# Optimization experiments

Hardware: AMD Instinct MI355X
Metric: run time of the kernel (lower is better)

The kernel has to match this reference:

```python
import jax
import jax.numpy as jnp
import numpy as np

KSIZE, STRIDE, RATE, FUSE_K, SCALE = 3, 1, 2, 3, 10.0
ESCAPE_NAN = 1e-4


def _same_pad(x, k, s):
    # replicates torch same_padding: asymmetric zero pad so out = ceil(H/s)
    H, W = x.shape[2], x.shape[3]
    oh, ow = -(-H // s), -(-W // s)
    ph = max(0, (oh - 1) * s + k - H)
    pw = max(0, (ow - 1) * s + k - W)
    return jnp.pad(x, ((0, 0), (0, 0), (ph // 2, ph - ph // 2), (pw // 2, pw - pw // 2)))


def _extract_patches(x, k, s):
    # torch extract_image_patches: -> [B, L, C, k, k] with L = out_h*out_w
    x = _same_pad(x, k, s)
    B, C, H, W = x.shape
    Ho, Wo = (H - k) // s + 1, (W - k) // s + 1
    slices = [x[:, :, i:i + Ho * s:s, j:j + Wo * s:s] for i in range(k) for j in range(k)]
    p = jnp.stack(slices, axis=2).reshape(B, C, k, k, Ho, Wo)
    return p.transpose(0, 4, 5, 1, 2, 3).reshape(B, Ho * Wo, C, k, k)


def _contextual_attention(f, b, mask):
    dn = ('NCHW', 'OIHW', 'NCHW')
    # raw background patches for the final deconv: k = 2*rate, stride = rate
    raw_pat = _extract_patches(b, 2 * RATE, RATE * STRIDE)  # [B, L, C, 4, 4]
    # nearest-neighbor 1/rate downsample (torch F.interpolate nearest, sf=0.5)
    f_ds = f[:, :, ::RATE, ::RATE]
    b_ds = b[:, :, ::RATE, ::RATE]
    m_ds = mask[:, :, ::RATE, ::RATE]
    B, C, Hf, Wf = f_ds.shape
    Hb, Wb = b_ds.shape[2], b_ds.shape[3]
    b_pat = _extract_patches(b_ds, KSIZE, STRIDE)  # [B, L, C, 3, 3], L = Hb*Wb
    m_pat = _extract_patches(m_ds, KSIZE, STRIDE)[0]  # [L, 1, 3, 3] (first sample only, as in torch)
    mm = (jnp.mean(m_pat, axis=(1, 2, 3)) == 0.0).astype(f.dtype)[None, :, None, None]  # [1, L, 1, 1]
    fuse_w = jnp.eye(FUSE_K, dtype=f.dtype).reshape(1, 1, FUSE_K, FUSE_K)

    def per_item(xi, wi, raw_wi):
        # xi: [C,Hf,Wf]; wi: [L,C,3,3]; raw_wi: [L,C,4,4]
        max_wi = jnp.sqrt(jnp.sum(wi * wi + ESCAPE_NAN, axis=(1, 2, 3), keepdims=True))
        wi_n = wi / max_wi
        # matching conv: scores [1, L, Hf, Wf]
        yi = jax.lax.conv_general_dilated(xi[None], wi_n, (1, 1), ((1, 1), (1, 1)), dimension_numbers=dn)
        # fuse: identity-diagonal 3x3 conv along (bg_idx, fg_idx) twice with transposes
        yi = yi.reshape(1, 1, Hb * Wb, Hf * Wf)
        yi = jax.lax.conv_general_dilated(yi, fuse_w, (1, 1), ((1, 1), (1, 1)), dimension_numbers=dn)
        yi = yi.reshape(Hb, Wb, Hf, Wf).transpose(1, 0, 3, 2).reshape(1, 1, Hb * Wb, Hf * Wf)
        yi = jax.lax.conv_general_dilated(yi, fuse_w, (1, 1), ((1, 1), (1, 1)), dimension_numbers=dn)
        yi = yi.reshape(Wb, Hb, Wf, Hf).transpose(1, 0, 3, 2).reshape(1, Hb * Wb, Hf, Wf)
        yi = yi * mm
        yi = jax.nn.softmax(yi * SCALE, axis=1) * mm
        # conv_transpose2d(yi, raw_wi[I=L,O=C], stride=rate, padding=1) / 4
        w2 = jnp.flip(raw_wi, (2, 3)).transpose(1, 0, 2, 3)  # [C, L, 4, 4]
        pad = 2 * RATE - 1 - 1  # k - 1 - torch_padding = 2
        out = jax.lax.conv_general_dilated(yi, w2, (1, 1), ((pad, pad), (pad, pad)),
                                           lhs_dilation=(RATE, RATE), dimension_numbers=dn) / 4.0
        return out[0]

    return jax.vmap(per_item)(f_ds, b_pat, raw_pat)  # [B, C, H, W]


def setup_inputs() -> dict:
    key = jax.random.key(0)
    k1, k2 = jax.random.split(key)
    B, C, H, W = 2, 128, 128, 128
    f = jax.random.normal(k1, (B, C, H, W), dtype=jnp.float32)
    b = jax.random.normal(k2, (B, C, H, W), dtype=jnp.float32)
    mask = jnp.zeros((B, 1, H, W), dtype=jnp.float32)
    return {"f": f, "b": b, "mask": mask}


def reference(f, b, mask):
    return _contextual_attention(f, b, mask)
```

## Files before the change

### kernel.cpp

```cpp
#include <hip/hip_runtime.h>
#include <math.h>

#define CDIM 128
#define HF   128
#define WF   128
#define NP   4096
#define NCHUNK 64

typedef __attribute__((ext_vector_type(8))) short short8;
typedef float __attribute__((ext_vector_type(4), aligned(16))) f4a16;
typedef float __attribute__((ext_vector_type(4), aligned(4)))  f4u;

__device__ inline ushort f2bf(float x) {
  union { float f; unsigned u; } v; v.f = x;
  unsigned r = v.u + 0x7fff + ((v.u >> 16) & 1);
  return (ushort)(r >> 16);
}
__device__ inline float bf2f(ushort h) {
  union { unsigned u; float f; } v; v.u = ((unsigned)h) << 16; return v.f;
}

__device__ inline void gl2lds16(const ushort* g, ushort* l) {
  __builtin_amdgcn_global_load_lds((const __attribute__((address_space(1))) void*)g,
                                   (__attribute__((address_space(3))) void*)l, 16, 0, 0);
}

__global__ __launch_bounds__(256) void k_prep(const float* __restrict__ f,
                                              const float* __restrict__ b,
                                              ushort* __restrict__ fcat,
                                              ushort* __restrict__ bcat) {
  int idx = blockIdx.x * 256 + threadIdx.x;
  int c = idx & 127, pos = idx >> 7;
  int x = pos & 63, y = pos >> 6;
  int src = c * 16384 + y * 256 + x * 2;
  float fv = f[src], bv = b[src];
  ushort fh = f2bf(fv); ushort fl = f2bf(fv - bf2f(fh));
  ushort bh = f2bf(bv); ushort bl = f2bf(bv - bf2f(bh));
  size_t base = (size_t)pos * 384;
  fcat[base + c] = fh; fcat[base + 128 + c] = fl; fcat[base + 256 + c] = fh;
  bcat[base + c] = bh; bcat[base + 128 + c] = bh; bcat[base + 256 + c] = bl;
}

__global__ __launch_bounds__(256) void k_mmp(const float* __restrict__ mask,
                                             float* __restrict__ mmp) {
  int a = blockIdx.x * 256 + threadIdx.x;
  int yb = a & 63, xb = a >> 6;
  float s = 0.f;
  for (int dy = -1; dy <= 1; ++dy)
    for (int dx = -1; dx <= 1; ++dx) {
      int y = yb + dy, x = xb + dx;
      if ((unsigned)y < 64u && (unsigned)x < 64u)
        s += mask[y * 256 + x * 2];
    }
  mmp[a] = (s == 0.0f) ? 1.0f : 0.0f;
}

__global__ __launch_bounds__(256) void k_sumsq(const float* __restrict__ b,
                                               float* __restrict__ s2) {
  int p = blockIdx.x * 256 + threadIdx.x;
  int x = p & 63, y = p >> 6;
  float s = 0.f;
  for (int c = 0; c < CDIM; ++c) {
    float v = b[c * 16384 + y * 256 + x * 2];
    s += v * v;
  }
  s2[p] = s;
}

__global__ __launch_bounds__(256) void k_norm(const float* __restrict__ s2,
                                              float* __restrict__ rnrm) {
  int p = blockIdx.x * 256 + threadIdx.x;
  int xb = p & 63, yb = p >> 6;
  float s = 0.f;
  for (int dy = -1; dy <= 1; ++dy)
    for (int dx = -1; dx <= 1; ++dx) {
      int y = yb + dy, x = xb + dx;
      if ((unsigned)y < 64u && (unsigned)x < 64u) s += s2[y * 64 + x];
    }
  rnrm[p] = rsqrtf(s + 1152.0f * 1.0e-4f);
}

__global__ __launch_bounds__(256) void k_mfma_gemm(const ushort* __restrict__ A,
                                                   const ushort* __restrict__ B,
                                                   float* __restrict__ Out,
                                                   int Kdim, int lda, int ldb, int ldo) {
  __shared__ ushort As[128 * 64];
  __shared__ ushort Bs[128 * 64];
  int tid = threadIdx.x;
  int wave = tid >> 6, lane = tid & 63;
  int quad = lane >> 4, l16 = lane & 15;
  int m0 = blockIdx.y * 128, n0 = blockIdx.x * 128;
  int wm = (wave >> 1) * 64, wn = (wave & 1) * 64;
  int srow = lane >> 3;
  int g = lane & 7;
  int gperm = (g ^ srow) * 8;

  f4a16 acc[4][4];
#pragma unroll
  for (int i = 0; i < 4; ++i)
#pragma unroll
    for (int j = 0; j < 4; ++j) acc[i][j] = (f4a16){0.f, 0.f, 0.f, 0.f};

  for (int k0 = 0; k0 < Kdim; k0 += 64) {
#pragma unroll
    for (int i = 0; i < 4; ++i) {
      int rbase = wave * 32 + i * 8;
      gl2lds16(A + (size_t)(m0 + rbase + srow) * lda + k0 + gperm, &As[rbase * 64]);
      gl2lds16(B + (size_t)(n0 + rbase + srow) * ldb + k0 + gperm, &Bs[rbase * 64]);
    }
    __syncthreads();
#pragma unroll
    for (int s = 0; s < 2; ++s) {
      short8 afrag[4], bfrag[4];
#pragma unroll
      for (int t = 0; t < 4; ++t) {
        int am = wm + t * 16 + l16;
        int ga = ((s * 4 + quad) ^ (am & 7)) * 8;
        afrag[t] = *reinterpret_cast<const short8*>(&As[am * 64 + ga]);
        int bn = wn + t * 16 + l16;
        int gb = ((s * 4 + quad) ^ (bn & 7)) * 8;
        bfrag[t] = *reinterpret_cast<const short8*>(&Bs[bn * 64 + gb]);
      }
#pragma unroll
      for (int i = 0; i < 4; ++i)
#pragma unroll
        for (int j = 0; j < 4; ++j)
          acc[i][j] = __builtin_amdgcn_mfma_f32_16x16x32_bf16(afrag[i], bfrag[j], acc[i][j], 0, 0, 0);
    }
    __syncthreads();
  }
#pragma unroll
  for (int i = 0; i < 4; ++i)
#pragma unroll
    for (int j = 0; j < 4; ++j)
#pragma unroll
      for (int r = 0; r < 4; ++r)
        Out[(size_t)(m0 + wm + i * 16 + quad * 4 + r) * ldo + (n0 + wn + j * 16 + l16)] = acc[i][j][r];
}

__global__ __launch_bounds__(256) void k_s0(const float* __restrict__ D,
                                            const float* __restrict__ rnrm,
                                            float* __restrict__ S0) {
  int p = blockIdx.x;
  int yb = p >> 6, xb = p & 63;
  float rp = rnrm[p];
  int t = threadIdx.x;
#pragma unroll
  for (int it = 0; it < 4; ++it) {
    int q = (it * 256 + t) << 2;
    int qy = q >> 6, qx = q & 63;
    f4a16 acc = (f4a16){0.f, 0.f, 0.f, 0.f};
#pragma unroll
    for (int dy = -1; dy <= 1; ++dy) {
      if ((unsigned)(yb + dy) >= 64u) continue;
      if ((unsigned)(qy + dy) >= 64u) continue;
#pragma unroll
      for (int dx = -1; dx <= 1; ++dx) {
        if ((unsigned)(xb + dx) >= 64u) continue;
        int delta = dy * 64 + dx;
        const float* base = D + (size_t)(p + delta) * 4096;
        f4u v;
        if (dx == -1 && qx == 0) {
          f4u r = *(const f4u*)(base + q + delta + 1);
          v = (f4u){0.f, r.x, r.y, r.z};
        } else {
          v = *(const f4u*)(base + q + delta);
          if (dx == 1 && qx == 60) v.w = 0.f;
        }
        acc += v;
      }
    }
    acc *= rp;
    *(f4a16*)(S0 + ((size_t)p << 12) + q) = acc;
  }
}

__global__ __launch_bounds__(256) void k_fuse1(const float* __restrict__ S0,
                                               float* __restrict__ Yp) {
  __shared__ float row[4160];
  int i = blockIdx.x;
  int t = threadIdx.x;
  const float* r0 = S0 + (size_t)(i - 1) * 4096;
  const float* r1 = S0 + (size_t)i * 4096;
  const float* r2 = S0 + (size_t)(i + 1) * 4096;
  bool up = (i > 0), dn = (i < 4095);
#pragma unroll
  for (int jj = 0; jj < 4; ++jj) {
    int j = (jj * 256 + t) << 2;
    f4u s = *(const f4u*)(r1 + j);
    if (up) {
      f4u a;
      if (j == 0) { f4u r = *(const f4u*)r0; a = (f4u){0.f, r.x, r.y, r.z}; }
      else a = *(const f4u*)(r0 + j - 1);
      s += a;
    }
    if (dn) {
      f4u d = *(const f4u*)(r2 + j + 1);
      if (j == 4092) d.w = 0.f;
      s += d;
    }
    int base = j + (j >> 6);
    row[base + 0] = s.x; row[base + 1] = s.y; row[base + 2] = s.z; row[base + 3] = s.w;
  }
  __syncthreads();
  int a = ((i & 63) << 6) | (i >> 6);
  float* orow = Yp + ((size_t)a << 12);
#pragma unroll
  for (int bb = 0; bb < 16; ++bb) {
    int b = bb * 256 + t;
    int jT = ((b & 63) << 6) | (b >> 6);
    orow[b] = row[jT + (jT >> 6)];
  }
}

__global__ __launch_bounds__(256) void k_smax_part(const float* __restrict__ Yp,
                                                   const float* __restrict__ mmp,
                                                   float* __restrict__ pm,
                                                   float* __restrict__ ps) {
  int v = (blockIdx.x * 256 + threadIdx.x) << 2;
  int chunk = blockIdx.y;
  f4a16 m = (f4a16){-1e30f, -1e30f, -1e30f, -1e30f};
  f4a16 s = (f4a16){0.f, 0.f, 0.f, 0.f};
  int u0 = chunk * (4096 / NCHUNK);
  for (int u = u0; u < u0 + (4096 / NCHUNK); ++u) {
    const float* row = Yp + ((size_t)u << 12);
    f4u tv = *(const f4u*)(row + v);
    if (u > 0) {
      f4u a;
      if (v == 0) { f4u r = *(const f4u*)(row - 4096); a = (f4u){0.f, r.x, r.y, r.z}; }
      else a = *(const f4u*)(row - 4096 + v - 1);
      tv += a;
    }
    if (u < 4095) {
      f4u d = *(const f4u*)(row + 4096 + v + 1);
      if (v == 4092) d.w = 0.f;
      tv += d;
    }
    float g = 10.0f * mmp[u];
    f4u x = tv * g;
#pragma unroll
    for (int l = 0; l < 4; ++l) {
      float xl = x[l];
      if (xl > m[l]) { s[l] = s[l] * __expf(m[l] - xl) + 1.0f; m[l] = xl; }
      else           { s[l] += __expf(xl - m[l]); }
    }
  }
  *(f4a16*)(pm + chunk * NP + v) = m;
  *(f4a16*)(ps + chunk * NP + v) = s;
}

__global__ __launch_bounds__(256) void k_smax_red(const float* __restrict__ pm,
                                                  const float* __restrict__ ps,
                                                  float* __restrict__ mcol,
                                                  float* __restrict__ rscol) {
  int v = (blockIdx.x * 256 + threadIdx.x) << 2;
  f4a16 m = *(const f4a16*)(pm + v);
  f4a16 s = *(const f4a16*)(ps + v);
  for (int ch = 1; ch < NCHUNK; ++ch) {
    f4a16 m2 = *(const f4a16*)(pm + ch * NP + v);
    f4a16 s2 = *(const f4a16*)(ps + ch * NP + v);
#pragma unroll
    for (int l = 0; l < 4; ++l) {
      if (m2[l] > m[l]) { s[l] = s[l] * __expf(m[l] - m2[l]) + s2[l]; m[l] = m2[l]; }
      else              { s[l] += s2[l] * __expf(m2[l] - m[l]); }
    }
  }
  *(f4a16*)(mcol + v) = m;
  f4a16 r;
#pragma unroll
  for (int l = 0; l < 4; ++l) r[l] = 1.0f / s[l];
  *(f4a16*)(rscol + v) = r;
}

__global__ __launch_bounds__(256) void k_attnT(const float* __restrict__ Yp,
                                               const float* __restrict__ mcol,
                                               const float* __restrict__ rscol,
                                               const float* __restrict__ mmp,
                                               ushort* __restrict__ AT) {
  __shared__ float T[64][65];
  int a0 = blockIdx.x * 64, b0 = blockIdx.y * 64;
  int t = threadIdx.x;
  int i = t >> 4, j4 = (t & 15) << 2;
#pragma unroll
  for (int r = 0; r < 4; ++r) {
    int al = r * 16 + i;
    int a = a0 + al;
    const float* row = Yp + ((size_t)a << 12);
    int b = b0 + j4;
    f4u y = *(const f4u*)(row + b);
    if (a > 0) {
      f4u u_;
      if (b == 0) { f4u rr = *(const f4u*)(row - 4096); u_ = (f4u){0.f, rr.x, rr.y, rr.z}; }
      else u_ = *(const f4u*)(row - 4096 + b - 1);
      y += u_;
    }
    if (a < 4095) {
      f4u d = *(const f4u*)(row + 4096 + b + 1);
      if (b == 4092) d.w = 0.f;
      y += d;
    }
    float g = mmp[a];
    f4a16 mc = *(const f4a16*)(mcol + b);
    f4a16 rs = *(const f4a16*)(rscol + b);
    f4u x = y * (10.0f * g);
#pragma unroll
    for (int l = 0; l < 4; ++l)
      T[al][j4 + l] = g * __expf(x[l] - mc[l]) * rs[l];
  }
  __syncthreads();
  int by0 = b0 >> 6;
  int c2 = (t & 31) << 1;
  int blb = t >> 5;
#pragma unroll
  for (int r = 0; r < 8; ++r) {
    int bl = r * 8 + blb;
    int q = bl * 64 + by0;
    unsigned lo = (unsigned)f2bf(T[c2][bl]);
    unsigned hi = (unsigned)f2bf(T[c2 + 1][bl]);
    *(unsigned*)(AT + ((size_t)q << 12) + a0 + c2) = lo | (hi << 16);
  }
}

__global__ __launch_bounds__(256) void k_vtT(const float* __restrict__ b,
                                             ushort* __restrict__ VtT) {
  __shared__ float T[64][65];
  int k2 = blockIdx.x;
  int t = threadIdx.x;
  int c = k2 >> 4, dy = (k2 >> 2) & 3, dx = k2 & 3;
  int px = t & 63;
#pragma unroll
  for (int r = 0; r < 16; ++r) {
    int py = r * 4 + (t >> 6);
    int sy = 2 * py + dy - 1, sx = 2 * px + dx - 1;
    float v = 0.f;
    if ((unsigned)sy < (unsigned)HF && (unsigned)sx < (unsigned)WF)
      v = b[c * 16384 + sy * 128 + sx];
    T[py][px] = v;
  }
  __syncthreads();
  ushort* orow = VtT + (size_t)k2 * 4096;
#pragma unroll
  for (int r = 0; r < 16; ++r) {
    int a = r * 256 + t;
    orow[a] = f2bf(T[a & 63][a >> 6]);
  }
}

__global__ __launch_bounds__(256) void k_scatter(const float* __restrict__ M,
                                                 float* __restrict__ out) {
  int idx = blockIdx.x * 256 + threadIdx.x;
  int ox = idx & 127, oy = (idx >> 7) & 127, c = idx >> 14;
  int qy[2], dyv[2], qx[2], dxv[2];
  if (oy & 1) { qy[0] = (oy - 1) >> 1; dyv[0] = 2; qy[1] = (oy + 1) >> 1; dyv[1] = 0; }
  else        { qy[0] = (oy >> 1) - 1; dyv[0] = 3; qy[1] = oy >> 1;       dyv[1] = 1; }
  if (ox & 1) { qx[0] = (ox - 1) >> 1; dxv[0] = 2; qx[1] = (ox + 1) >> 1; dxv[1] = 0; }
  else        { qx[0] = (ox >> 1) - 1; dxv[0] = 3; qx[1] = ox >> 1;       dxv[1] = 1; }
  float s = 0.f;
#pragma unroll
  for (int i = 0; i < 2; ++i) {
    if ((unsigned)qy[i] >= 64u) continue;
#pragma unroll
    for (int j = 0; j < 2; ++j) {
      if ((unsigned)qx[j] >= 64u) continue;
      int k = c * 16 + dyv[i] * 4 + dxv[j];
      s += M[(size_t)k * NP + qy[i] * 64 + qx[j]];
    }
  }
  out[idx] = 0.25f * s;
}

extern "C" void kernel_launch(void* const* d_in, const int* in_sizes, int n_in,
                              void* d_out, int out_size, void* d_ws, size_t ws_size,
                              hipStream_t stream) {
  const float* f_all = (const float*)d_in[0];
  const float* b_all = (const float*)d_in[1];
  const float* m_all = (const float*)d_in[2];
  float* out = (float*)d_out;

  float* ws = (float*)d_ws;
  float* bufD = ws;
  float* bufS = ws + 16777216;
  ushort* fcat = (ushort*)bufS;
  ushort* bcat = (ushort*)(bufS + 786432);
  float* S0  = bufS;
  float* Yp  = bufD;
  ushort* AT  = (ushort*)bufS;
  ushort* VtT = (ushort*)(bufS + 8388608);
  float* Mbuf = bufD;
  float* smalls = ws + 2 * 16777216;
  float* s2    = smalls;
  float* rnrm  = s2 + 4096;
  float* mmp   = rnrm + 4096;
  float* pm    = mmp + 4096;
  float* ps    = pm + NCHUNK * NP;
  float* mcol  = ps + NCHUNK * NP;
  float* rscol = mcol + 4096;

  for (int it = 0; it < 2; ++it) {
    const float* f = f_all + (size_t)it * CDIM * HF * WF;
    const float* b = b_all + (size_t)it * CDIM * HF * WF;
    const float* mk = m_all + (size_t)it * HF * WF;
    float* o = out + (size_t)it * CDIM * HF * WF;

    k_prep<<<2048, 256, 0, stream>>>(f, b, fcat, bcat);
    k_mmp<<<16, 256, 0, stream>>>(mk, mmp);
    k_sumsq<<<16, 256, 0, stream>>>(b, s2);
    k_norm<<<16, 256, 0, stream>>>(s2, rnrm);
    k_mfma_gemm<<<dim3(32, 32), 256, 0, stream>>>(bcat, fcat, bufD, 384, 384, 384, NP);
    k_s0<<<4096, 256, 0, stream>>>(bufD, rnrm, S0);
    k_fuse1<<<4096, 256, 0, stream>>>(S0, Yp);
    k_smax_part<<<dim3(4, NCHUNK), 256, 0, stream>>>(Yp, mmp, pm, ps);
    k_smax_red<<<4, 256, 0, stream>>>(pm, ps, mcol, rscol);
    k_attnT<<<dim3(64, 64), 256, 0, stream>>>(Yp, mcol, rscol, mmp, AT);
    k_vtT<<<2048, 256, 0, stream>>>(b, VtT);
    k_mfma_gemm<<<dim3(32, 16), 256, 0, stream>>>(VtT, AT, Mbuf, NP, NP, NP, NP);
    k_scatter<<<8192, 256, 0, stream>>>(Mbuf, o);
  }
}
```

Measured before the change: 755.0 us.

## Batch both items into one pipeline via grid z-dimension

```diff
diff --git a/kernel.cpp b/kernel.cpp
--- a/kernel.cpp
+++ b/kernel.cpp
@@ -7,6 +7,8 @@
 #define NP   4096
 #define NCHUNK 64
 
+#define ITEM_WS (2 * 16777216 + 3 * 4096 + 2 * (NCHUNK * NP) + 2 * 4096)
+
 typedef __attribute__((ext_vector_type(8))) short short8;
 typedef float __attribute__((ext_vector_type(4), aligned(16))) f4a16;
 typedef float __attribute__((ext_vector_type(4), aligned(4)))  f4u;
@@ -28,7 +30,11 @@
 __global__ __launch_bounds__(256) void k_prep(const float* __restrict__ f,
                                               const float* __restrict__ b,
                                               ushort* __restrict__ fcat,
-                                              ushort* __restrict__ bcat) {
+                                              ushort* __restrict__ bcat,
+                                              size_t zsF, size_t zsW) {
+  size_t zW = (size_t)blockIdx.z * zsW;
+  f += (size_t)blockIdx.z * zsF; b += (size_t)blockIdx.z * zsF;
+  fcat += 2 * zW; bcat += 2 * zW;
   int idx = blockIdx.x * 256 + threadIdx.x;
   int c = idx & 127, pos = idx >> 7;
   int x = pos & 63, y = pos >> 6;
@@ -42,7 +48,9 @@
 }
 
 __global__ __launch_bounds__(256) void k_mmp(const float* __restrict__ mask,
-                                             float* __restrict__ mmp) {
+                                             float* __restrict__ mmp,
+                                             size_t zsM, size_t zsW) {
+  mask += (size_t)blockIdx.z * zsM; mmp += (size_t)blockIdx.z * zsW;
   int a = blockIdx.x * 256 + threadIdx.x;
   int yb = a & 63, xb = a >> 6;
   float s = 0.f;
@@ -56,7 +64,9 @@
 }
 
 __global__ __launch_bounds__(256) void k_sumsq(const float* __restrict__ b,
-                                               float* __restrict__ s2) {
+                                               float* __restrict__ s2,
+                                               size_t zsF, size_t zsW) {
+  b += (size_t)blockIdx.z * zsF; s2 += (size_t)blockIdx.z * zsW;
   int p = blockIdx.x * 256 + threadIdx.x;
   int x = p & 63, y = p >> 6;
   float s = 0.f;
@@ -68,7 +78,9 @@
 }
 
 __global__ __launch_bounds__(256) void k_norm(const float* __restrict__ s2,
-                                              float* __restrict__ rnrm) {
+                                              float* __restrict__ rnrm,
+                                              size_t zsW) {
+  s2 += (size_t)blockIdx.z * zsW; rnrm += (size_t)blockIdx.z * zsW;
   int p = blockIdx.x * 256 + threadIdx.x;
   int xb = p & 63, yb = p >> 6;
   float s = 0.f;
@@ -83,7 +95,10 @@
 __global__ __launch_bounds__(256) void k_mfma_gemm(const ushort* __restrict__ A,
                                                    const ushort* __restrict__ B,
                                                    float* __restrict__ Out,
-                                                   int Kdim, int lda, int ldb, int ldo) {
+                                                   int Kdim, int lda, int ldb, int ldo,
+                                                   size_t zsW) {
+  size_t zW = (size_t)blockIdx.z * zsW;
+  A += 2 * zW; B += 2 * zW; Out += zW;
   __shared__ ushort As[128 * 64];
   __shared__ ushort Bs[128 * 64];
   int tid = threadIdx.x;
@@ -140,7 +155,10 @@
 
 __global__ __launch_bounds__(256) void k_s0(const float* __restrict__ D,
                                             const float* __restrict__ rnrm,
-                                            float* __restrict__ S0) {
+                                            float* __restrict__ S0,
+                                            size_t zsW) {
+  size_t zW = (size_t)blockIdx.z * zsW;
+  D += zW; rnrm += zW; S0 += zW;
   int p = blockIdx.x;
   int yb = p >> 6, xb = p & 63;
   float rp = rnrm[p];
@@ -176,7 +194,10 @@
 }
 
 __global__ __launch_bounds__(256) void k_fuse1(const float* __restrict__ S0,
-                                               float* __restrict__ Yp) {
+                                               float* __restrict__ Yp,
+                                               size_t zsW) {
+  size_t zW = (size_t)blockIdx.z * zsW;
+  S0 += zW; Yp += zW;
   __shared__ float row[4160];
   int i = blockIdx.x;
   int t = threadIdx.x;
@@ -216,7 +237,10 @@
 __global__ __launch_bounds__(256) void k_smax_part(const float* __restrict__ Yp,
                                                    const float* __restrict__ mmp,
                                                    float* __restrict__ pm,
-                                                   float* __restrict__ ps) {
+                                                   float* __restrict__ ps,
+                                                   size_t zsW) {
+  size_t zW = (size_t)blockIdx.z * zsW;
+  Yp += zW; mmp += zW; pm += zW; ps += zW;
   int v = (blockIdx.x * 256 + threadIdx.x) << 2;
   int chunk = blockIdx.y;
   f4a16 m = (f4a16){-1e30f, -1e30f, -1e30f, -1e30f};
@@ -252,7 +276,10 @@
 __global__ __launch_bounds__(256) void k_smax_red(const float* __restrict__ pm,
                                                   const float* __restrict__ ps,
                                                   float* __restrict__ mcol,
-                                                  float* __restrict__ rscol) {
+                                                  float* __restrict__ rscol,
+                                                  size_t zsW) {
+  size_t zW = (size_t)blockIdx.z * zsW;
+  pm += zW; ps += zW; mcol += zW; rscol += zW;
   int v = (blockIdx.x * 256 + threadIdx.x) << 2;
   f4a16 m = *(const f4a16*)(pm + v);
   f4a16 s = *(const f4a16*)(ps + v);
@@ -276,7 +303,10 @@
                                                const float* __restrict__ mcol,
                                                const float* __restrict__ rscol,
                                                const float* __restrict__ mmp,
-                                               ushort* __restrict__ AT) {
+                                               ushort* __restrict__ AT,
+                                               size_t zsW) {
+  size_t zW = (size_t)blockIdx.z * zsW;
+  Yp += zW; mcol += zW; rscol += zW; mmp += zW; AT += 2 * zW;
   __shared__ float T[64][65];
   int a0 = blockIdx.x * 64, b0 = blockIdx.y * 64;
   int t = threadIdx.x;
@@ -322,7 +352,9 @@
 }
 
 __global__ __launch_bounds__(256) void k_vtT(const float* __restrict__ b,
-                                             ushort* __restrict__ VtT) {
+                                             ushort* __restrict__ VtT,
+                                             size_t zsF, size_t zsW) {
+  b += (size_t)blockIdx.z * zsF; VtT += 2 * (size_t)blockIdx.z * zsW;
   __shared__ float T[64][65];
   int k2 = blockIdx.x;
   int t = threadIdx.x;
@@ -347,7 +379,9 @@
 }
 
 __global__ __launch_bounds__(256) void k_scatter(const float* __restrict__ M,
-                                                 float* __restrict__ out) {
+                                                 float* __restrict__ out,
+                                                 size_t zsW, size_t zsF) {
+  M += (size_t)blockIdx.z * zsW; out += (size_t)blockIdx.z * zsF;
   int idx = blockIdx.x * 256 + threadIdx.x;
   int ox = idx & 127, oy = (idx >> 7) & 127, c = idx >> 14;
   int qy[2], dyv[2], qx[2], dxv[2];
@@ -369,15 +403,9 @@
   out[idx] = 0.25f * s;
 }
 
-extern "C" void kernel_launch(void* const* d_in, const int* in_sizes, int n_in,
-                              void* d_out, int out_size, void* d_ws, size_t ws_size,
-                              hipStream_t stream) {
-  const float* f_all = (const float*)d_in[0];
-  const float* b_all = (const float*)d_in[1];
-  const float* m_all = (const float*)d_in[2];
-  float* out = (float*)d_out;
-
-  float* ws = (float*)d_ws;
+static void run_pipeline(const float* f, const float* b, const float* mk, float* out,
+                         float* ws, int nz, size_t zsF, size_t zsM, size_t zsW,
+                         hipStream_t stream) {
   float* bufD = ws;
   float* bufS = ws + 16777216;
   ushort* fcat = (ushort*)bufS;
@@ -396,24 +424,39 @@
   float* mcol  = ps + NCHUNK * NP;
   float* rscol = mcol + 4096;
 
-  for (int it = 0; it < 2; ++it) {
-    const float* f = f_all + (size_t)it * CDIM * HF * WF;
-    const float* b = b_all + (size_t)it * CDIM * HF * WF;
-    const float* mk = m_all + (size_t)it * HF * WF;
-    float* o = out + (size_t)it * CDIM * HF * WF;
-
-    k_prep<<<2048, 256, 0, stream>>>(f, b, fcat, bcat);
-    k_mmp<<<16, 256, 0, stream>>>(mk, mmp);
-    k_sumsq<<<16, 256, 0, stream>>>(b, s2);
-    k_norm<<<16, 256, 0, stream>>>(s2, rnrm);
-    k_mfma_gemm<<<dim3(32, 32), 256, 0, stream>>>(bcat, fcat, bufD, 384, 384, 384, NP);
-    k_s0<<<4096, 256, 0, stream>>>(bufD, rnrm, S0);
-    k_fuse1<<<4096, 256, 0, stream>>>(S0, Yp);
-    k_smax_part<<<dim3(4, NCHUNK), 256, 0, stream>>>(Yp, mmp, pm, ps);
-    k_smax_red<<<4, 256, 0, stream>>>(pm, ps, mcol, rscol);
-    k_attnT<<<dim3(64, 64), 256, 0, stream>>>(Yp, mcol, rscol, mmp, AT);
-    k_vtT<<<2048, 256, 0, stream>>>(b, VtT);
-    k_mfma_gemm<<<dim3(32, 16), 256, 0, stream>>>(VtT, AT, Mbuf, NP, NP, NP, NP);
-    k_scatter<<<8192, 256, 0, stream>>>(Mbuf, o);
-  }
-}
+  k_prep<<<dim3(2048, 1, nz), 256, 0, stream>>>(f, b, fcat, bcat, zsF, zsW);
+  k_mmp<<<dim3(16, 1, nz), 256, 0, stream>>>(mk, mmp, zsM, zsW);
+  k_sumsq<<<dim3(16, 1, nz), 256, 0, stream>>>(b, s2, zsF, zsW);
+  k_norm<<<dim3(16, 1, nz), 256, 0, stream>>>(s2, rnrm, zsW);
+  k_mfma_gemm<<<dim3(32, 32, nz), 256, 0, stream>>>(bcat, fcat, bufD, 384, 384, 384, NP, zsW);
+  k_s0<<<dim3(4096, 1, nz), 256, 0, stream>>>(bufD, rnrm, S0, zsW);
+  k_fuse1<<<dim3(4096, 1, nz), 256, 0, stream>>>(S0, Yp, zsW);
+  k_smax_part<<<dim3(4, NCHUNK, nz), 256, 0, stream>>>(Yp, mmp, pm, ps, zsW);
+  k_smax_red<<<dim3(4, 1, nz), 256, 0, stream>>>(pm, ps, mcol, rscol, zsW);
+  k_attnT<<<dim3(64, 64, nz), 256, 0, stream>>>(Yp, mcol, rscol, mmp, AT, zsW);
+  k_vtT<<<dim3(2048, 1, nz), 256, 0, stream>>>(b, VtT, zsF, zsW);
+  k_mfma_gemm<<<dim3(32, 16, nz), 256, 0, stream>>>(VtT, AT, Mbuf, NP, NP, NP, NP, zsW);
+  k_scatter<<<dim3(8192, 1, nz), 256, 0, stream>>>(Mbuf, out, zsW, zsF);
+}
+
+extern "C" void kernel_launch(void* const* d_in, const int* in_sizes, int n_in,
+                              void* d_out, int out_size, void* d_ws, size_t ws_size,
+                              hipStream_t stream) {
+  const float* f_all = (const float*)d_in[0];
+  const float* b_all = (const float*)d_in[1];
+  const float* m_all = (const float*)d_in[2];
+  float* out = (float*)d_out;
+  float* ws = (float*)d_ws;
+
+  const size_t zsF = (size_t)CDIM * HF * WF;
+  const size_t zsM = (size_t)HF * WF;
+
+  if (ws_size >= (size_t)2 * ITEM_WS * sizeof(float)) {
+    run_pipeline(f_all, b_all, m_all, out, ws, 2, zsF, zsM, (size_t)ITEM_WS, stream);
+  } else {
+    for (int it = 0; it < 2; ++it) {
+      run_pipeline(f_all + it * zsF, b_all + it * zsF, m_all + it * zsM,
+                   out + it * zsF, ws, 1, 0, 0, 0, stream);
+    }
+  }
+}
```

New measurement: 763.9 us. Within noise of the previous version (+1.2%).

## Fuse prep kernels and split-K the output GEMM across two z slices

Applied to the files above, without the earlier changes.

```diff
diff --git a/kernel.cpp b/kernel.cpp
--- a/kernel.cpp
+++ b/kernel.cpp
@@ -28,7 +28,8 @@
 __global__ __launch_bounds__(256) void k_prep(const float* __restrict__ f,
                                               const float* __restrict__ b,
                                               ushort* __restrict__ fcat,
-                                              ushort* __restrict__ bcat) {
+                                              ushort* __restrict__ bcat,
+                                              float* __restrict__ s2) {
   int idx = blockIdx.x * 256 + threadIdx.x;
   int c = idx & 127, pos = idx >> 7;
   int x = pos & 63, y = pos >> 6;
@@ -39,51 +40,52 @@
   size_t base = (size_t)pos * 384;
   fcat[base + c] = fh; fcat[base + 128 + c] = fl; fcat[base + 256 + c] = fh;
   bcat[base + c] = bh; bcat[base + 128 + c] = bh; bcat[base + 256 + c] = bl;
-}
-
-__global__ __launch_bounds__(256) void k_mmp(const float* __restrict__ mask,
-                                             float* __restrict__ mmp) {
-  int a = blockIdx.x * 256 + threadIdx.x;
-  int yb = a & 63, xb = a >> 6;
-  float s = 0.f;
-  for (int dy = -1; dy <= 1; ++dy)
-    for (int dx = -1; dx <= 1; ++dx) {
-      int y = yb + dy, x = xb + dx;
-      if ((unsigned)y < 64u && (unsigned)x < 64u)
-        s += mask[y * 256 + x * 2];
-    }
-  mmp[a] = (s == 0.0f) ? 1.0f : 0.0f;
-}
-
-__global__ __launch_bounds__(256) void k_sumsq(const float* __restrict__ b,
-                                               float* __restrict__ s2) {
-  int p = blockIdx.x * 256 + threadIdx.x;
-  int x = p & 63, y = p >> 6;
-  float s = 0.f;
-  for (int c = 0; c < CDIM; ++c) {
-    float v = b[c * 16384 + y * 256 + x * 2];
-    s += v * v;
-  }
-  s2[p] = s;
-}
-
-__global__ __launch_bounds__(256) void k_norm(const float* __restrict__ s2,
-                                              float* __restrict__ rnrm) {
-  int p = blockIdx.x * 256 + threadIdx.x;
-  int xb = p & 63, yb = p >> 6;
-  float s = 0.f;
-  for (int dy = -1; dy <= 1; ++dy)
-    for (int dx = -1; dx <= 1; ++dx) {
-      int y = yb + dy, x = xb + dx;
-      if ((unsigned)y < 64u && (unsigned)x < 64u) s += s2[y * 64 + x];
-    }
-  rnrm[p] = rsqrtf(s + 1152.0f * 1.0e-4f);
+  float sq = bv * bv;
+#pragma unroll
+  for (int off = 32; off; off >>= 1) sq += __shfl_down(sq, off);
+  __shared__ float wsum[4];
+  if ((threadIdx.x & 63) == 0) wsum[threadIdx.x >> 6] = sq;
+  __syncthreads();
+  if (threadIdx.x == 0) s2[blockIdx.x * 2]     = wsum[0] + wsum[1];
+  if (threadIdx.x == 1) s2[blockIdx.x * 2 + 1] = wsum[2] + wsum[3];
+}
+
+__global__ __launch_bounds__(256) void k_mmpnorm(const float* __restrict__ mask,
+                                                 const float* __restrict__ s2,
+                                                 float* __restrict__ mmp,
+                                                 float* __restrict__ rnrm) {
+  int bx = blockIdx.x, t = threadIdx.x;
+  if (bx < 16) {
+    int a = bx * 256 + t;
+    int yb = a & 63, xb = a >> 6;
+    float s = 0.f;
+    for (int dy = -1; dy <= 1; ++dy)
+      for (int dx = -1; dx <= 1; ++dx) {
+        int y = yb + dy, x = xb + dx;
+        if ((unsigned)y < 64u && (unsigned)x < 64u)
+          s += mask[y * 256 + x * 2];
+      }
+    mmp[a] = (s == 0.0f) ? 1.0f : 0.0f;
+  } else {
+    int p = (bx - 16) * 256 + t;
+    int xb = p & 63, yb = p >> 6;
+    float s = 0.f;
+    for (int dy = -1; dy <= 1; ++dy)
+      for (int dx = -1; dx <= 1; ++dx) {
+        int y = yb + dy, x = xb + dx;
+        if ((unsigned)y < 64u && (unsigned)x < 64u) s += s2[y * 64 + x];
+      }
+    rnrm[p] = rsqrtf(s + 1152.0f * 1.0e-4f);
+  }
 }
 
 __global__ __launch_bounds__(256) void k_mfma_gemm(const ushort* __restrict__ A,
                                                    const ushort* __restrict__ B,
                                                    float* __restrict__ Out,
-                                                   int Kdim, int lda, int ldb, int ldo) {
+                                                   int Kdim, int lda, int ldb, int ldo,
+                                                   size_t kz, size_t oz) {
+  A += (size_t)blockIdx.z * kz; B += (size_t)blockIdx.z * kz;
+  Out += (size_t)blockIdx.z * oz;
   __shared__ ushort As[128 * 64];
   __shared__ ushort Bs[128 * 64];
   int tid = threadIdx.x;
@@ -348,6 +350,7 @@
 
 __global__ __launch_bounds__(256) void k_scatter(const float* __restrict__ M,
                                                  float* __restrict__ out) {
+  const float* M1 = M + 8388608;
   int idx = blockIdx.x * 256 + threadIdx.x;
   int ox = idx & 127, oy = (idx >> 7) & 127, c = idx >> 14;
   int qy[2], dyv[2], qx[2], dxv[2];
@@ -362,8 +365,8 @@
 #pragma unroll
     for (int j = 0; j < 2; ++j) {
       if ((unsigned)qx[j] >= 64u) continue;
-      int k = c * 16 + dyv[i] * 4 + dxv[j];
-      s += M[(size_t)k * NP + qy[i] * 64 + qx[j]];
+      size_t off = (size_t)(c * 16 + dyv[i] * 4 + dxv[j]) * NP + qy[i] * 64 + qx[j];
+      s += M[off] + M1[off];
     }
   }
   out[idx] = 0.25f * s;
@@ -396,24 +399,26 @@
   float* mcol  = ps + NCHUNK * NP;
   float* rscol = mcol + 4096;
 
+  const size_t zsF = (size_t)CDIM * HF * WF;
+  const size_t zsM = (size_t)HF * WF;
+
   for (int it = 0; it < 2; ++it) {
-    const float* f = f_all + (size_t)it * CDIM * HF * WF;
-    const float* b = b_all + (size_t)it * CDIM * HF * WF;
-    const float* mk = m_all + (size_t)it * HF * WF;
-    float* o = out + (size_t)it * CDIM * HF * WF;
-
-    k_prep<<<2048, 256, 0, stream>>>(f, b, fcat, bcat);
-    k_mmp<<<16, 256, 0, stream>>>(mk, mmp);
-    k_sumsq<<<16, 256, 0, stream>>>(b, s2);
-    k_norm<<<16, 256, 0, stream>>>(s2, rnrm);
-    k_mfma_gemm<<<dim3(32, 32), 256, 0, stream>>>(bcat, fcat, bufD, 384, 384, 384, NP);
+    const float* f = f_all + it * zsF;
+    const float* b = b_all + it * zsF;
+    const float* mk = m_all + it * zsM;
+    float* o = out + it * zsF;
+
+    k_prep<<<2048, 256, 0, stream>>>(f, b, fcat, bcat, s2);
+    k_mmpnorm<<<32, 256, 0, stream>>>(mk, s2, mmp, rnrm);
+    k_mfma_gemm<<<dim3(32, 32, 1), 256, 0, stream>>>(bcat, fcat, bufD, 384, 384, 384, NP, 0, 0);
     k_s0<<<4096, 256, 0, stream>>>(bufD, rnrm, S0);
     k_fuse1<<<4096, 256, 0, stream>>>(S0, Yp);
     k_smax_part<<<dim3(4, NCHUNK), 256, 0, stream>>>(Yp, mmp, pm, ps);
     k_smax_red<<<4, 256, 0, stream>>>(pm, ps, mcol, rscol);
     k_attnT<<<dim3(64, 64), 256, 0, stream>>>(Yp, mcol, rscol, mmp, AT);
     k_vtT<<<2048, 256, 0, stream>>>(b, VtT);
-    k_mfma_gemm<<<dim3(32, 16), 256, 0, stream>>>(VtT, AT, Mbuf, NP, NP, NP, NP);
+    k_mfma_gemm<<<dim3(32, 16, 2), 256, 0, stream>>>(VtT, AT, Mbuf, 2048, NP, NP, NP,
+                                                     2048, 8388608);
     k_scatter<<<8192, 256, 0, stream>>>(Mbuf, o);
   }
 }
```

Result: no change. 752.4 us (-0.4%).
